# Performance work log

Hardware: AMD Instinct MI355X
Metric: run time of the kernel (lower is better)

## Reference

```python
import jax, jax.numpy as jnp
import numpy as np

N_NODES = 50000
N_EDGES = 800000
IN_CH = 128
OUT_CH = 64
SELF_LOOP_W = 2.0  # improved=True in GCNConv


def setup_inputs() -> dict:
    key = jax.random.key(0)
    k1, k2, k3, k4 = jax.random.split(key, 4)
    x = jax.random.normal(k1, (N_NODES, IN_CH), dtype=jnp.float32)
    edge_index = jax.random.randint(k2, (2, N_EDGES), 0, N_NODES, dtype=jnp.int64)
    edge_weight = jax.random.uniform(k3, (N_EDGES,), dtype=jnp.float32)
    W = jax.random.normal(k4, (IN_CH, OUT_CH), dtype=jnp.float32) / np.sqrt(IN_CH)
    b = jnp.zeros((OUT_CH,), dtype=jnp.float32)
    return {"x": x, "edge_index": edge_index, "edge_weight": edge_weight, "W": W, "b": b}


def reference(x, edge_index, edge_weight, W, b):
    # Only the first GCNConv layer runs (the torch loop returns after k=0).
    N = x.shape[0]
    row, col = edge_index[0], edge_index[1]  # source, target

    # gcn_norm with add_self_loops=True, improved=True (fill value 2.0)
    loop_idx = jnp.arange(N, dtype=edge_index.dtype)
    row_f = jnp.concatenate([row, loop_idx])
    col_f = jnp.concatenate([col, loop_idx])
    ew_f = jnp.concatenate([edge_weight, jnp.full((N,), SELF_LOOP_W, dtype=edge_weight.dtype)])

    deg = jax.ops.segment_sum(ew_f, col_f, num_segments=N)          # [N]
    dinv = jnp.where(deg > 0, jax.lax.rsqrt(deg), 0.0)
    norm = dinv[row_f] * ew_f * dinv[col_f]                          # [E+N]

    # linear transform then normalized sparse aggregation
    xw = x @ W                                                       # [N, out]
    msg = norm[:, None] * xw[row_f]                                  # [E+N, out] gather
    out = jax.ops.segment_sum(msg, col_f, num_segments=N)           # [N, out] scatter-add
    return out + b
```

## Files before the change

kernel.cpp:

```cpp
#include <hip/hip_runtime.h>

constexpr int N    = 50000;
constexpr int E    = 800000;
constexpr int CIN  = 128;
constexpr int COUT = 64;
constexpr float SELF_LOOP_W = 2.0f;

constexpr int NB   = (N + 63) / 64;
constexpr int CAP  = 1536;
constexpr int EPB  = 4096;
constexpr int PBLK = (E + EPB - 1) / EPB;

typedef float          vfloat4  __attribute__((ext_vector_type(4)));
typedef int            vint2    __attribute__((ext_vector_type(2)));
typedef unsigned short vushort4 __attribute__((ext_vector_type(4)));

__device__ __forceinline__ unsigned short f2bf(float f) {
    unsigned int u = __float_as_uint(f);
    u += 0x7FFFu + ((u >> 16) & 1u);
    return (unsigned short)(u >> 16);
}
__device__ __forceinline__ float bf2f(unsigned short h) {
    return __uint_as_float(((unsigned int)h) << 16);
}

__global__ void init_kernel(int* __restrict__ bcur) {
    int i = blockIdx.x * blockDim.x + threadIdx.x;
    if (i < NB) bcur[i] = i * CAP;
}

__global__ __launch_bounds__(512) void partition_kernel(const int* __restrict__ row,
                                                        const int* __restrict__ col,
                                                        const float* __restrict__ ew,
                                                        int* __restrict__ bcur,
                                                        vint2* __restrict__ pk) {
    __shared__ int lhist[NB];
    __shared__ int lbase[NB];
    const int t  = threadIdx.x;
    const int e0 = blockIdx.x * EPB;

    for (int i = t; i < NB; i += 512) lhist[i] = 0;
    __syncthreads();

    #pragma unroll
    for (int k = 0; k < EPB / 512; ++k) {
        int e = e0 + k * 512 + t;
        if (e < E) atomicAdd(&lhist[col[e] >> 6], 1);
    }
    __syncthreads();

    for (int i = t; i < NB; i += 512) {
        int h = lhist[i];
        lbase[i] = (h > 0) ? atomicAdd(&bcur[i], h) : 0;
    }
    __syncthreads();
    for (int i = t; i < NB; i += 512) lhist[i] = 0;
    __syncthreads();

    #pragma unroll
    for (int k = 0; k < EPB / 512; ++k) {
        int e = e0 + k * 512 + t;
        if (e < E) {
            int c   = col[e];
            int bkt = c >> 6;
            int p = lbase[bkt] + atomicAdd(&lhist[bkt], 1);
            if (p < (bkt + 1) * CAP) {
                vint2 v;
                v.x = row[e] | ((c & 63) << 20);
                v.y = __float_as_int(ew[e]);
                pk[p] = v;
            }
        }
    }
}

__global__ __launch_bounds__(256) void deg_kernel(const int* __restrict__ bcur,
                                                  const vint2* __restrict__ pk,
                                                  float* __restrict__ dinv) {
    __shared__ float ldeg[64];
    const int t    = threadIdx.x;
    const int b    = blockIdx.x;
    const int base = b * CAP;
    const int cnt  = min(bcur[b] - base, CAP);

    if (t < 64) ldeg[t] = 0.f;
    __syncthreads();
    for (int j = t; j < cnt; j += 256) {
        vint2 v = pk[base + j];
        atomicAdd(&ldeg[(v.x >> 20) & 63], __int_as_float(v.y));
    }
    __syncthreads();
    int node = b * 64 + t;
    if (t < 64 && node < N) dinv[node] = rsqrtf(SELF_LOOP_W + ldeg[t]);
}

__global__ __launch_bounds__(256) void xw_kernel(const float* __restrict__ x,
                                                 const float* __restrict__ W,
                                                 float* __restrict__ xw,
                                                 unsigned short* __restrict__ xwh) {
    __shared__ __align__(16) float xs[64][132];

    const int t    = threadIdx.x;
    const int base = blockIdx.x * 64;

    #pragma unroll
    for (int i = 0; i < 8; ++i) {
        int f4  = i * 256 + t;
        int r   = f4 >> 5;
        int c4  = f4 & 31;
        int node = base + r;
        if (node >= N) node = N - 1;
        vfloat4 v = *(const vfloat4*)(x + (size_t)node * CIN + c4 * 4);
        *(vfloat4*)&xs[r][c4 * 4] = v;
    }
    __syncthreads();

    const int tc = t & 15;
    const int tn = t >> 4;

    float acc[4][4];
    #pragma unroll
    for (int i = 0; i < 4; ++i)
        #pragma unroll
        for (int j = 0; j < 4; ++j) acc[i][j] = 0.f;

    const float* Wp = W + tc * 4;
    #pragma unroll 8
    for (int k = 0; k < CIN; ++k) {
        vfloat4 bv = *(const vfloat4*)(Wp + (size_t)k * COUT);
        float a0 = xs[tn * 4 + 0][k];
        float a1 = xs[tn * 4 + 1][k];
        float a2 = xs[tn * 4 + 2][k];
        float a3 = xs[tn * 4 + 3][k];
        #pragma unroll
        for (int j = 0; j < 4; ++j) {
            acc[0][j] += a0 * bv[j];
            acc[1][j] += a1 * bv[j];
            acc[2][j] += a2 * bv[j];
            acc[3][j] += a3 * bv[j];
        }
    }

    #pragma unroll
    for (int i = 0; i < 4; ++i) {
        int node = base + tn * 4 + i;
        if (node >= N) continue;
        vfloat4 xv;
        vushort4 hv;
        #pragma unroll
        for (int j = 0; j < 4; ++j) { xv[j] = acc[i][j]; hv[j] = f2bf(acc[i][j]); }
        *(vfloat4*) (xw  + (size_t)node * COUT + tc * 4) = xv;
        *(vushort4*)(xwh + (size_t)node * COUT + tc * 4) = hv;
    }
}

__global__ __launch_bounds__(512) void aggregate_kernel(const int* __restrict__ bcur,
                                                        const vint2* __restrict__ pk,
                                                        const float* __restrict__ dinv,
                                                        const float* __restrict__ xw,
                                                        const unsigned short* __restrict__ xwh,
                                                        const float* __restrict__ bias,
                                                        float* __restrict__ out) {
    __shared__ int   rawx[CAP];
    __shared__ float rawn[CAP];
    __shared__ int   s_r[CAP];
    __shared__ float s_n[CAP];
    __shared__ int   lhist[64], lofs[64], lcur[64];

    const int t    = threadIdx.x;
    const int lane = t & 63;
    const int wv   = t >> 6;
    const int b    = blockIdx.x;
    const int base = b * CAP;
    const int cnt  = min(bcur[b] - base, CAP);

    if (t < 64) lhist[t] = 0;
    __syncthreads();

    for (int j = t; j < cnt; j += 512) {
        vint2 v = pk[base + j];
        rawx[j] = v.x;
        rawn[j] = __int_as_float(v.y) * dinv[v.x & 0xFFFFF];
        atomicAdd(&lhist[(v.x >> 20) & 63], 1);
    }
    __syncthreads();

    if (t < 64) {
        int v = lhist[t];
        int s = v;
        #pragma unroll
        for (int d = 1; d < 64; d <<= 1) {
            int u = __shfl_up(s, d);
            if (lane >= d) s += u;
        }
        lofs[t] = s - v;
        lcur[t] = s - v;
    }
    __syncthreads();

    for (int j = t; j < cnt; j += 512) {
        int xv = rawx[j];
        int p  = atomicAdd(&lcur[(xv >> 20) & 63], 1);
        s_r[p] = xv & 0xFFFFF;
        s_n[p] = rawn[j];
    }
    __syncthreads();

    float bl = bias[lane];
    for (int nd = wv; nd < 64; nd += 8) {
        int node = b * 64 + nd;
        if (node >= N) continue;
        int s0 = lofs[nd];
        int e0 = s0 + lhist[nd];
        float acc = 0.f;
        int i = s0;
        for (; i + 8 <= e0; i += 8) {
            int r[8]; float n[8], v[8];
            #pragma unroll
            for (int u = 0; u < 8; ++u) { r[u] = s_r[i + u]; n[u] = s_n[i + u]; }
            #pragma unroll
            for (int u = 0; u < 8; ++u)
                v[u] = bf2f(xwh[(size_t)r[u] * COUT + lane]);
            #pragma unroll
            for (int u = 0; u < 8; ++u) acc += n[u] * v[u];
        }
        for (; i < e0; ++i)
            acc += s_n[i] * bf2f(xwh[(size_t)s_r[i] * COUT + lane]);

        float dc = dinv[node];
        float xv = xw[(size_t)node * COUT + lane];
        out[(size_t)node * COUT + lane] =
            dc * acc + SELF_LOOP_W * dc * dc * xv + bl;
    }
}

extern "C" void kernel_launch(void* const* d_in, const int* in_sizes, int n_in,
                              void* d_out, int out_size, void* d_ws, size_t ws_size,
                              hipStream_t stream) {
    const float* x  = (const float*)d_in[0];
    const int*   ei = (const int*)d_in[1];
    const float* ew = (const float*)d_in[2];
    const float* W  = (const float*)d_in[3];
    const float* b  = (const float*)d_in[4];
    float* out = (float*)d_out;

    float*          xw   = (float*)d_ws;
    float*          dinv = xw + (size_t)N * COUT;
    int*            bcur = (int*)(dinv + N);
    vint2*          pk   = (vint2*)(bcur + NB + 2);
    unsigned short* xwh  = (unsigned short*)(pk + (size_t)NB * CAP);

    const int* rowp = ei;
    const int* colp = ei + E;

    init_kernel     <<<(NB + 255) / 256, 256, 0, stream>>>(bcur);
    partition_kernel<<<PBLK, 512, 0, stream>>>(rowp, colp, ew, bcur, pk);
    xw_kernel       <<<NB, 256, 0, stream>>>(x, W, xw, xwh);
    deg_kernel      <<<NB, 256, 0, stream>>>(bcur, pk, dinv);
    aggregate_kernel<<<NB, 512, 0, stream>>>(bcur, pk, dinv, xw, xwh, b, out);
}
```

Before: 153.2 us.

## Stage partition records in LDS and drop fp32 xw buffer

The partition kernel now reads each edge's row, col and weight once, packs the record and its bucket into shared memory, and scatters from LDS in the second pass instead of re-reading global memory. EPB is halved so the staging buffers fit in LDS. The fp32 copy of xw is removed: xw_kernel writes only the bf16 version, and the self-loop term in aggregation reads bf16. This cuts global reads and writes, at the cost of slightly lower precision on the self-loop term and twice as many partition blocks doing bucket atomics.

```diff
diff --git a/kernel.cpp b/kernel.cpp
--- a/kernel.cpp
+++ b/kernel.cpp
@@ -8,7 +8,7 @@
 
 constexpr int NB   = (N + 63) / 64;
 constexpr int CAP  = 1536;
-constexpr int EPB  = 4096;
+constexpr int EPB  = 2048;
 constexpr int PBLK = (E + EPB - 1) / EPB;
 
 typedef float          vfloat4  __attribute__((ext_vector_type(4)));
@@ -34,18 +34,32 @@
                                                         const float* __restrict__ ew,
                                                         int* __restrict__ bcur,
                                                         vint2* __restrict__ pk) {
-    __shared__ int lhist[NB];
-    __shared__ int lbase[NB];
+    __shared__ vint2 srec[EPB];
+    __shared__ short sbkt[EPB];
+    __shared__ int   lhist[NB];
+    __shared__ int   lbase[NB];
+
     const int t  = threadIdx.x;
     const int e0 = blockIdx.x * EPB;
+    const int m  = min(EPB, E - e0);
 
     for (int i = t; i < NB; i += 512) lhist[i] = 0;
     __syncthreads();
 
     #pragma unroll
     for (int k = 0; k < EPB / 512; ++k) {
-        int e = e0 + k * 512 + t;
-        if (e < E) atomicAdd(&lhist[col[e] >> 6], 1);
+        int j = k * 512 + t;
+        int e = e0 + j;
+        if (j < m) {
+            int c   = col[e];
+            int bkt = c >> 6;
+            vint2 v;
+            v.x = row[e] | ((c & 63) << 20);
+            v.y = __float_as_int(ew[e]);
+            srec[j] = v;
+            sbkt[j] = (short)bkt;
+            atomicAdd(&lhist[bkt], 1);
+        }
     }
     __syncthreads();
 
@@ -59,17 +73,12 @@
 
     #pragma unroll
     for (int k = 0; k < EPB / 512; ++k) {
-        int e = e0 + k * 512 + t;
-        if (e < E) {
-            int c   = col[e];
-            int bkt = c >> 6;
+        int j = k * 512 + t;
+        if (j < m) {
+            int bkt = sbkt[j];
             int p = lbase[bkt] + atomicAdd(&lhist[bkt], 1);
-            if (p < (bkt + 1) * CAP) {
-                vint2 v;
-                v.x = row[e] | ((c & 63) << 20);
-                v.y = __float_as_int(ew[e]);
-                pk[p] = v;
-            }
+            if (p < (bkt + 1) * CAP)
+                pk[p] = srec[j];
         }
     }
 }
@@ -96,7 +105,6 @@
 
 __global__ __launch_bounds__(256) void xw_kernel(const float* __restrict__ x,
                                                  const float* __restrict__ W,
-                                                 float* __restrict__ xw,
                                                  unsigned short* __restrict__ xwh) {
     __shared__ __align__(16) float xs[64][132];
 
@@ -145,11 +153,9 @@
     for (int i = 0; i < 4; ++i) {
         int node = base + tn * 4 + i;
         if (node >= N) continue;
-        vfloat4 xv;
         vushort4 hv;
         #pragma unroll
-        for (int j = 0; j < 4; ++j) { xv[j] = acc[i][j]; hv[j] = f2bf(acc[i][j]); }
-        *(vfloat4*) (xw  + (size_t)node * COUT + tc * 4) = xv;
+        for (int j = 0; j < 4; ++j) hv[j] = f2bf(acc[i][j]);
         *(vushort4*)(xwh + (size_t)node * COUT + tc * 4) = hv;
     }
 }
@@ -157,7 +163,6 @@
 __global__ __launch_bounds__(512) void aggregate_kernel(const int* __restrict__ bcur,
                                                         const vint2* __restrict__ pk,
                                                         const float* __restrict__ dinv,
-                                                        const float* __restrict__ xw,
                                                         const unsigned short* __restrict__ xwh,
                                                         const float* __restrict__ bias,
                                                         float* __restrict__ out) {
@@ -228,7 +233,7 @@
             acc += s_n[i] * bf2f(xwh[(size_t)s_r[i] * COUT + lane]);
 
         float dc = dinv[node];
-        float xv = xw[(size_t)node * COUT + lane];
+        float xv = bf2f(xwh[(size_t)node * COUT + lane]);
         out[(size_t)node * COUT + lane] =
             dc * acc + SELF_LOOP_W * dc * dc * xv + bl;
     }
@@ -244,18 +249,17 @@
     const float* b  = (const float*)d_in[4];
     float* out = (float*)d_out;
 
-    float*          xw   = (float*)d_ws;
-    float*          dinv = xw + (size_t)N * COUT;
+    unsigned short* xwh  = (unsigned short*)d_ws;
+    float*          dinv = (float*)(xwh + (size_t)N * COUT);
     int*            bcur = (int*)(dinv + N);
     vint2*          pk   = (vint2*)(bcur + NB + 2);
-    unsigned short* xwh  = (unsigned short*)(pk + (size_t)NB * CAP);
 
     const int* rowp = ei;
     const int* colp = ei + E;
 
     init_kernel     <<<(NB + 255) / 256, 256, 0, stream>>>(bcur);
     partition_kernel<<<PBLK, 512, 0, stream>>>(rowp, colp, ew, bcur, pk);
-    xw_kernel       <<<NB, 256, 0, stream>>>(x, W, xw, xwh);
+    xw_kernel       <<<NB, 256, 0, stream>>>(x, W, xwh);
     deg_kernel      <<<NB, 256, 0, stream>>>(bcur, pk, dinv);
-    aggregate_kernel<<<NB, 512, 0, stream>>>(bcur, pk, dinv, xw, xwh, b, out);
-}
+    aggregate_kernel<<<NB, 512, 0, stream>>>(bcur, pk, dinv, xwh, b, out);
+}
```

Result: no change. 156.1 us (+1.9%).
